# Kernel tuning notes

Hardware: AMD Instinct MI355X
Metric: run time of the kernel (lower is better)

## Reference

```python
import jax, jax.numpy as jnp
import numpy as np

B, T, L = 16, 2048, 512
CH, H_ENC, H_DEC, ATTN_SZ, VOCAB, EMB = 256, 100, 200, 50, 6, 64


def _conv1d(x, k):
    # x: [B,T,Cin], k: [K,Cin,Cout], SAME padding, stride 1
    return jax.lax.conv_general_dilated(x, k, (1,), 'SAME', dimension_numbers=('NWC', 'WIO', 'NWC'))


def _lstm_step(x, c, h, W, b):
    # TF BasicLSTMCell: gates ordered [i, j, f, o], forget_bias = 1.0
    z = jnp.concatenate([x, h], -1) @ W + b
    i, j, f, o = jnp.split(z, 4, -1)
    nc = c * jax.nn.sigmoid(f + 1.0) + jax.nn.sigmoid(i) * jnp.tanh(j)
    nh = jnp.tanh(nc) * jax.nn.sigmoid(o)
    return nc, nh


def _run_lstm(xs, lengths, W, b, hidden):
    # dynamic_rnn semantics: beyond sequence_length, state held, output zeroed
    Bn, Tn, _ = xs.shape
    mask = (jnp.arange(Tn)[:, None] < lengths[None, :])[..., None]  # [T,B,1]

    def step(carry, inp):
        c, h = carry
        x, m = inp
        nc, nh = _lstm_step(x, c, h, W, b)
        c = jnp.where(m, nc, c)
        h = jnp.where(m, nh, h)
        return (c, h), jnp.where(m, nh, 0.0)

    init = (jnp.zeros((Bn, hidden), xs.dtype), jnp.zeros((Bn, hidden), xs.dtype))
    (c, h), outs = jax.lax.scan(step, init, (jnp.swapaxes(xs, 0, 1), mask))
    return jnp.swapaxes(outs, 0, 1), c, h


def _reverse_seq(x, lengths):
    # tf.reverse_sequence along time axis
    t = jnp.arange(x.shape[1])[None, :]
    idx = jnp.where(t < lengths[:, None], lengths[:, None] - 1 - t, t)
    return jnp.take_along_axis(x, idx[..., None], axis=1)


def setup_inputs():
    key = jax.random.key(0)
    ks = jax.random.split(key, 16)
    s = 0.05
    f32 = jnp.float32
    return {
        'signals': jax.random.normal(ks[0], (B, T), f32),
        'embeddings': jax.random.normal(ks[1], (VOCAB, EMB), f32) * s,
        'conv1_k': jax.random.normal(ks[2], (1, 1, CH), f32) * s,
        'conv1a_k': jax.random.normal(ks[3], (1, 1, CH), f32) * s,
        'conv1a_b': jnp.zeros((CH,), f32),
        'conv2_k': jax.random.normal(ks[4], (3, CH, CH), f32) * s,
        'conv3_k': jax.random.normal(ks[5], (1, CH, CH), f32) * s,
        'W_fwd': jax.random.normal(ks[6], (CH + H_ENC, 4 * H_ENC), f32) * s,
        'b_fwd': jnp.zeros((4 * H_ENC,), f32),
        'W_bwd': jax.random.normal(ks[7], (CH + H_ENC, 4 * H_ENC), f32) * s,
        'b_bwd': jnp.zeros((4 * H_ENC,), f32),
        'W_dec': jax.random.normal(ks[8], (EMB + ATTN_SZ + H_DEC, 4 * H_DEC), f32) * s,
        'b_dec': jnp.zeros((4 * H_DEC,), f32),
        'W_mem': jax.random.normal(ks[9], (H_DEC, H_DEC), f32) * s,
        'W_attn': jax.random.normal(ks[10], (2 * H_DEC, ATTN_SZ), f32) * s,
        'W_out': jax.random.normal(ks[11], (ATTN_SZ, VOCAB), f32) * s,
        'labels': jax.random.randint(ks[12], (B, L), 0, 4),
        'sig_length': jax.random.randint(ks[13], (B,), T // 2, T + 1),
        'base_length': jax.random.randint(ks[14], (B,), L // 2, L + 1),
    }


def reference(signals, embeddings, conv1_k, conv1a_k, conv1a_b, conv2_k, conv3_k,
              W_fwd, b_fwd, W_bwd, b_bwd, W_dec, b_dec, W_mem, W_attn, W_out,
              labels, sig_length, base_length):
    # ---- resBlock ----
    x = signals[..., None]                       # [B,T,1]
    c1 = _conv1d(x, conv1_k)                     # no bias
    c1a = _conv1d(x, conv1a_k) + conv1a_b        # with bias (shortcut)
    c3 = _conv1d(_conv1d(c1, conv2_k), conv3_k)
    feat = jax.nn.relu(c3 + c1a)                 # [B,T,256]

    # ---- bidirectional encoder ----
    fwd_out, cf, hf = _run_lstm(feat, sig_length, W_fwd, b_fwd, H_ENC)
    bwd_out, cb, hb = _run_lstm(_reverse_seq(feat, sig_length), sig_length, W_bwd, b_bwd, H_ENC)
    bwd_out = _reverse_seq(bwd_out, sig_length)
    memory = jnp.concatenate([fwd_out, bwd_out], -1)   # [B,T,200]
    c0 = jnp.concatenate([cf, cb], -1)                 # [B,200]
    h0 = jnp.concatenate([hf, hb], -1)

    # ---- Luong attention decoder (teacher forcing) ----
    keys = jnp.einsum('btd,de->bte', memory, W_mem)    # memory_layer (no bias)
    mem_mask = jnp.arange(T)[None, :] < sig_length[:, None]
    neg = jnp.finfo(memory.dtype).min
    emb = embeddings[labels]                            # [B,L,64]

    def dec_step(carry, x_t):
        c, h, attn = carry
        nc, nh = _lstm_step(jnp.concatenate([x_t, attn], -1), c, h, W_dec, b_dec)
        score = jnp.einsum('bd,btd->bt', nh, keys)
        align = jax.nn.softmax(jnp.where(mem_mask, score, neg), axis=-1)
        ctx = jnp.einsum('bt,btd->bd', align, memory)
        new_attn = jnp.concatenate([nh, ctx], -1) @ W_attn   # attention_layer (no bias)
        return (nc, nh, new_attn), new_attn @ W_out          # output Dense(6, no bias)

    attn0 = jnp.zeros((B, ATTN_SZ), memory.dtype)
    _, logits = jax.lax.scan(dec_step, (c0, h0, attn0), jnp.swapaxes(emb, 0, 1))
    logits = jnp.swapaxes(logits, 0, 1)                      # [B,L,6]
    dec_mask = (jnp.arange(L)[None, :] < base_length[:, None])[..., None]
    return jnp.where(dec_mask, logits, jnp.zeros((), logits.dtype))
```

## Files before the change

### kernel.cpp

```cpp
#include <hip/hip_runtime.h>

#define B_ 16
#define T_ 2048
#define L_ 512
#define HD 200
#define AT 50

__device__ __forceinline__ float rcp_(float x){ return __builtin_amdgcn_rcpf(x); }
__device__ __forceinline__ float sigf(float x){ return rcp_(1.f + __expf(-x)); }
__device__ __forceinline__ float tanhf_(float x){
  x = fminf(15.f, fmaxf(-15.f, x));
  float e = __expf(-2.f*x);
  return (1.f - e) * rcp_(1.f + e);
}
__device__ __forceinline__ unsigned bf16u(float v){
  unsigned u = __float_as_uint(v);
  u += 0x7FFFu + ((u >> 16) & 1u);
  return u >> 16;
}
__device__ __forceinline__ unsigned long long pkvs(float v, unsigned s){
  return (unsigned long long)__float_as_uint(v) | ((unsigned long long)s << 32);
}

__global__ void k_prep(const float* __restrict__ conv1, const float* __restrict__ conv1a,
                       const float* __restrict__ conv2, const float* __restrict__ conv3,
                       float* __restrict__ E)
{
  __shared__ float K2s[3*256];
  int tid = threadIdx.x;
  int k = tid >> 8, co = tid & 255;
  float a = 0.f;
  for (int ci = 0; ci < 256; ++ci)
    a = fmaf(conv1[ci], conv2[(k*256 + ci)*256 + co], a);
  K2s[k*256 + co] = a;
  __syncthreads();
  float b2 = 0.f;
  for (int ci = 0; ci < 256; ++ci)
    b2 = fmaf(K2s[k*256 + ci], conv3[ci*256 + co], b2);
  if (k == 1) b2 += conv1a[co];
  E[k*256 + co] = b2;
}

__global__ void k_feat(const float* __restrict__ sig, const float* __restrict__ E,
                       const float* __restrict__ c1ab, float* __restrict__ feat)
{
  int idx = blockIdx.x*256 + threadIdx.x;
  int row = idx >> 6;
  int c4  = (idx & 63) * 4;
  int t = row & (T_-1);
  float sm = (t > 0)     ? sig[row-1] : 0.f;
  float s0 = sig[row];
  float sp = (t < T_-1)  ? sig[row+1] : 0.f;
  float4 e0 = *(const float4*)&E[0*256 + c4];
  float4 e1 = *(const float4*)&E[1*256 + c4];
  float4 e2 = *(const float4*)&E[2*256 + c4];
  float4 bb = *(const float4*)&c1ab[c4];
  float4 r;
  r.x = fmaxf(0.f, fmaf(sm, e0.x, fmaf(s0, e1.x, fmaf(sp, e2.x, bb.x))));
  r.y = fmaxf(0.f, fmaf(sm, e0.y, fmaf(s0, e1.y, fmaf(sp, e2.y, bb.y))));
  r.z = fmaxf(0.f, fmaf(sm, e0.z, fmaf(s0, e1.z, fmaf(sp, e2.z, bb.z))));
  r.w = fmaxf(0.f, fmaf(sm, e0.w, fmaf(s0, e1.w, fmaf(sp, e2.w, bb.w))));
  *(float4*)&feat[(size_t)row*256 + c4] = r;
}

__global__ __launch_bounds__(256)
void k_gemm(const float* __restrict__ A, const float* __restrict__ B,
            const float* __restrict__ bias, float* __restrict__ C,
            int M, int N, int K, int ldb)
{
  __shared__ float As[16][132];
  __shared__ float Bs[16][68];
  int row0 = blockIdx.x*128, col0 = blockIdx.y*64;
  int tid = threadIdx.x;
  int tm = tid >> 4, tn = tid & 15;
  float acc[8][4] = {};
  for (int k0 = 0; k0 < K; k0 += 16){
    #pragma unroll
    for (int i = 0; i < 8; ++i){
      int e = tid + i*256;
      int m = e >> 4, kk = e & 15;
      float v = 0.f;
      if (k0 + kk < K) v = A[(size_t)(row0+m)*K + k0 + kk];
      As[kk][m] = v;
    }
    #pragma unroll
    for (int i = 0; i < 4; ++i){
      int e = tid + i*256;
      int n = e & 63, kb = e >> 6;
      float w = 0.f;
      if (k0 + kb < K && col0 + n < N) w = B[(size_t)(k0+kb)*ldb + col0 + n];
      Bs[kb][n] = w;
    }
    __syncthreads();
    #pragma unroll
    for (int kk = 0; kk < 16; ++kk){
      float a[8], bv[4];
      *(float4*)&a[0] = *(const float4*)&As[kk][tm*8];
      *(float4*)&a[4] = *(const float4*)&As[kk][tm*8+4];
      *(float4*)&bv[0] = *(const float4*)&Bs[kk][tn*4];
      #pragma unroll
      for (int i = 0; i < 8; ++i)
        #pragma unroll
        for (int j = 0; j < 4; ++j)
          acc[i][j] = fmaf(a[i], bv[j], acc[i][j]);
    }
    __syncthreads();
  }
  #pragma unroll
  for (int i = 0; i < 8; ++i){
    int r = row0 + tm*8 + i;
    #pragma unroll
    for (int j = 0; j < 4; ++j){
      int cc = col0 + tn*4 + j;
      if (cc < N) C[(size_t)r*N + cc] = acc[i][j] + (bias ? bias[cc] : 0.f);
    }
  }
}

__global__ void k_permW(const float* __restrict__ Wf, const float* __restrict__ bf,
                        const float* __restrict__ Wb, const float* __restrict__ bb,
                        float* __restrict__ WpF, float* __restrict__ WpB)
{
  int idx = blockIdx.x*256 + threadIdx.x;
  if (idx >= 2*357*400) return;
  int w = idx / (357*400), r = idx - w*(357*400);
  int j = r / 400, col = r - j*400;
  int src = (col & 3)*100 + (col >> 2);
  const float* W = w ? Wb : Wf; const float* bs = w ? bb : bf;
  float v = (j < 356) ? W[j*400 + src] : bs[src];
  (w ? WpB : WpF)[j*400 + col] = v;
}

__global__ __launch_bounds__(512, 1)
void k_encoder(const float* __restrict__ xprojF, const float* __restrict__ xprojB,
               const float* __restrict__ WpF, const float* __restrict__ WpB,
               const int* __restrict__ sig_len, float* __restrict__ memory,
               float* __restrict__ c0h0, int dirParam)
{
  int dir = dirParam, b = blockIdx.x;
  const float* xp = dir ? xprojB : xprojF;
  const float* Wp = dir ? WpB : WpF;
  int tid = threadIdx.x;
  bool act = tid < 400;
  int col = act ? tid : (tid - 400);
  int u = tid >> 2, gq = tid & 3;
  __shared__ __align__(16) float h2[2][104];
  float4 Uv[25];
  #pragma unroll
  for (int j4 = 0; j4 < 25; ++j4){
    Uv[j4].x = Wp[(256 + 4*j4 + 0)*400 + col];
    Uv[j4].y = Wp[(256 + 4*j4 + 1)*400 + col];
    Uv[j4].z = Wp[(256 + 4*j4 + 2)*400 + col];
    Uv[j4].w = Wp[(256 + 4*j4 + 3)*400 + col];
  }
  if (tid < 100) h2[0][tid] = 0.f;
  int len = sig_len[b];
  float c = 0.f, hfin = 0.f;
  int ta = dir ? (len-1) : 0;
  float xb0 = xp[((size_t)(b*T_ + ta))*400 + col];
  int tb_ = dir ? (len-2) : 1;
  float xb1 = xp[((size_t)(b*T_ + tb_))*400 + col];
  for (int step = 0; step < len; ++step){
    __syncthreads();
    int tn = dir ? (len-3-step) : (step+2);
    tn = tn < 0 ? 0 : (tn > T_-1 ? T_-1 : tn);
    float xn = xp[((size_t)(b*T_ + tn))*400 + col];
    const float* hb = h2[step & 1];
    float a0 = xb0, a1 = 0.f, a2 = 0.f, a3 = 0.f;
    #pragma unroll
    for (int j4 = 0; j4 < 25; ++j4){
      float4 h4 = *(const float4*)&hb[j4*4];
      a0 = fmaf(h4.x, Uv[j4].x, a0);
      a1 = fmaf(h4.y, Uv[j4].y, a1);
      a2 = fmaf(h4.z, Uv[j4].z, a2);
      a3 = fmaf(h4.w, Uv[j4].w, a3);
    }
    float z = (a0+a1)+(a2+a3);
    float v0 = z, v1 = __shfl_xor(z, 1);
    float v2 = __shfl_xor(v0, 2), v3 = __shfl_xor(v1, 2);
    float tA  = (gq&1) ? v1 : v0, tB  = (gq&1) ? v3 : v2;
    float tA2 = (gq&1) ? v0 : v1, tB2 = (gq&1) ? v2 : v3;
    float zi = (gq&2) ? tB  : tA;
    float zj = (gq&2) ? tB2 : tA2;
    float zf = (gq&2) ? tA  : tB;
    float zo = (gq&2) ? tA2 : tB2;
    c = c*sigf(zf + 1.f) + sigf(zi)*tanhf_(zj);
    float nh = tanhf_(c)*sigf(zo);
    hfin = nh;
    if (act && gq == 0){
      int t = dir ? (len-1-step) : step;
      h2[(step+1)&1][u] = nh;
      memory[((size_t)(b*T_ + t))*200 + dir*100 + u] = nh;
    }
    xb0 = xb1; xb1 = xn;
  }
  if (act && gq == 0){
    c0h0[b*400 + dir*100 + u]       = c;
    c0h0[b*400 + 200 + dir*100 + u] = hfin;
  }
  int total = (T_ - len)*100;
  for (int i = tid; i < total; i += 512){
    int t = len + i/100;
    int k = i - (i/100)*100;
    memory[((size_t)(b*T_ + t))*200 + dir*100 + k] = 0.f;
  }
}

__global__ void k_gather(const float* __restrict__ emb, const int* __restrict__ labels,
                         float* __restrict__ dA)
{
  int idx = blockIdx.x*256 + threadIdx.x;
  int i = idx >> 6, e = idx & 63;
  dA[(size_t)i*64 + e] = emb[labels[i]*64 + e];
}

__global__ void k_dec_init(unsigned long long* __restrict__ nhb,
                           unsigned long long* __restrict__ parts,
                           unsigned* __restrict__ flags, unsigned fval,
                           float* __restrict__ out)
{
  int idx = blockIdx.x*256 + threadIdx.x;
  if (idx < B_*L_*6) out[idx] = 0.f;
  if (idx < B_*HD) nhb[idx] = 0ull;
  if (idx < B_*16*112) parts[idx] = 0ull;
  if (idx < 32) flags[idx] = fval;
}

#define DEC_LDS 141440
#define TCH 128

__global__ __launch_bounds__(512, 1)
void k_fused(const float* __restrict__ xprojF, const float* __restrict__ xprojB,
             const float* __restrict__ WpF, const float* __restrict__ WpB,
             float* __restrict__ memG, float* c0h0,
             const float* __restrict__ W_mem, const float* __restrict__ W_attn,
             const float* __restrict__ decx, const float* __restrict__ W_dec,
             const float* __restrict__ W_out,
             const int* __restrict__ sig_len, const int* __restrict__ base_len,
             unsigned long long* nhb, unsigned long long* partials,
             unsigned* flags, int encInside,
             float* __restrict__ out)
{
  int blk = blockIdx.x;
  int b = (blk & 7) | (((blk >> 3) & 1) << 3);
  int g = blk >> 4;
  int tid = threadIdx.x;
  int u0 = g * 13;
  int nu = (HD - u0 < 13) ? (HD - u0) : 13;
  int t0 = g * TCH;

  extern __shared__ char smem[];
  uint2* keyP  = (uint2*)(smem);
  float* memAL = (float*)(smem + 51616);
  float* Uld   = (float*)(smem + 77216);
  float* Wa1s  = (float*)(smem + 129216);
  float* WoutL = (float*)(smem + 131824);
  float* nhF   = (float*)(smem + 133024);
  float* spL   = (float*)(smem + 133856);
  float* wL    = (float*)(smem + 135904);
  float* cpL   = (float*)(smem + 136416);
  float* apL   = (float*)(smem + 138080);
  float* zp8   = (float*)(smem + 138288);
  float* zpA   = (float*)(smem + 139952);
  float* attnL = (float*)(smem + 140784);
  float* SL    = (float*)(smem + 140992);
  float* ctxR  = (float*)(smem + 141000);
  float* apR   = (float*)(smem + 141208);

  if (encInside && g < 2){
    int dir = g;
    const float* xp = dir ? xprojB : xprojF;
    const float* Wp = dir ? WpB : WpF;
    float* h2 = spL;
    bool act = tid < 400;
    int col = act ? tid : (tid - 400);
    int u = tid >> 2, gq = tid & 3;
    float4 Uv[25];
    #pragma unroll
    for (int j4 = 0; j4 < 25; ++j4){
      Uv[j4].x = Wp[(256 + 4*j4 + 0)*400 + col];
      Uv[j4].y = Wp[(256 + 4*j4 + 1)*400 + col];
      Uv[j4].z = Wp[(256 + 4*j4 + 2)*400 + col];
      Uv[j4].w = Wp[(256 + 4*j4 + 3)*400 + col];
    }
    if (tid < 104) { h2[tid] = 0.f; h2[104 + tid] = 0.f; }
    int len = sig_len[b];
    float c = 0.f, hfin = 0.f;
    int ta = dir ? (len-1) : 0;
    float xb0 = xp[((size_t)(b*T_ + ta))*400 + col];
    int tb_ = dir ? (len-2) : 1;
    float xb1 = xp[((size_t)(b*T_ + tb_))*400 + col];
    for (int step = 0; step < len; ++step){
      __syncthreads();
      int tn = dir ? (len-3-step) : (step+2);
      tn = tn < 0 ? 0 : (tn > T_-1 ? T_-1 : tn);
      float xn = xp[((size_t)(b*T_ + tn))*400 + col];
      const float* hb = h2 + (step & 1)*104;
      float a0 = xb0, a1 = 0.f, a2 = 0.f, a3 = 0.f;
      #pragma unroll
      for (int j4 = 0; j4 < 25; ++j4){
        float4 h4 = *(const float4*)&hb[j4*4];
        a0 = fmaf(h4.x, Uv[j4].x, a0);
        a1 = fmaf(h4.y, Uv[j4].y, a1);
        a2 = fmaf(h4.z, Uv[j4].z, a2);
        a3 = fmaf(h4.w, Uv[j4].w, a3);
      }
      float z = (a0+a1)+(a2+a3);
      float v0 = z, v1 = __shfl_xor(z, 1);
      float v2 = __shfl_xor(v0, 2), v3 = __shfl_xor(v1, 2);
      float tA  = (gq&1) ? v1 : v0, tB  = (gq&1) ? v3 : v2;
      float tA2 = (gq&1) ? v0 : v1, tB2 = (gq&1) ? v2 : v3;
      float zi = (gq&2) ? tB  : tA;
      float zj = (gq&2) ? tB2 : tA2;
      float zf = (gq&2) ? tA  : tB;
      float zo = (gq&2) ? tA2 : tB2;
      c = c*sigf(zf + 1.f) + sigf(zi)*tanhf_(zj);
      float nh = tanhf_(c)*sigf(zo);
      hfin = nh;
      if (act && gq == 0){
        int t = dir ? (len-1-step) : step;
        h2[((step+1)&1)*104 + u] = nh;
        memG[((size_t)(b*T_ + t))*200 + dir*100 + u] = nh;
      }
      xb0 = xb1; xb1 = xn;
    }
    if (act && gq == 0){
      c0h0[b*400 + dir*100 + u]       = c;
      c0h0[b*400 + 200 + dir*100 + u] = hfin;
    }
    int total = (T_ - len)*100;
    for (int i = tid; i < total; i += 512){
      int t = len + i/100;
      int k = i - (i/100)*100;
      memG[((size_t)(b*T_ + t))*200 + dir*100 + k] = 0.f;
    }
    __syncthreads();
    if (tid == 0){
      __builtin_amdgcn_fence(__ATOMIC_RELEASE, "agent");
      __hip_atomic_store(&flags[b*2 + dir], 1u,
                         __ATOMIC_RELAXED, __HIP_MEMORY_SCOPE_AGENT);
    }
  }

  if (encInside){
    if (tid == 0){
      while (__hip_atomic_load(&flags[b*2+0], __ATOMIC_RELAXED, __HIP_MEMORY_SCOPE_AGENT) == 0u)
        __builtin_amdgcn_s_sleep(8);
      while (__hip_atomic_load(&flags[b*2+1], __ATOMIC_RELAXED, __HIP_MEMORY_SCOPE_AGENT) == 0u)
        __builtin_amdgcn_s_sleep(8);
      __builtin_amdgcn_fence(__ATOMIC_ACQUIRE, "agent");
    }
    __syncthreads();
  }

  unsigned* stg = (unsigned*)Uld;
  for (int i = tid; i < TCH*100; i += 512){
    int t = i / 100, p2 = i - (i/100)*100;
    float2 mv = *(const float2*)&memG[((size_t)(b*T_ + t0 + t))*200 + 2*p2];
    stg[i] = bf16u(mv.x) | (bf16u(mv.y) << 16);
  }
  __syncthreads();
  for (int i = tid; i < TCH*50; i += 512){
    int t = i / 50, q = i - (i/50)*50;
    int d = q*4;
    const unsigned* mrow = stg + t*100;
    float ax = 0.f, ay = 0.f, az = 0.f, aw = 0.f;
    for (int p2 = 0; p2 < 100; ++p2){
      unsigned mm = mrow[p2];
      float m0 = __uint_as_float(mm << 16);
      float m1 = __uint_as_float(mm & 0xFFFF0000u);
      float4 w0 = *(const float4*)&W_mem[(size_t)(2*p2)*200 + d];
      float4 w1 = *(const float4*)&W_mem[(size_t)(2*p2+1)*200 + d];
      ax = fmaf(m0, w0.x, fmaf(m1, w1.x, ax));
      ay = fmaf(m0, w0.y, fmaf(m1, w1.y, ay));
      az = fmaf(m0, w0.z, fmaf(m1, w1.z, az));
      aw = fmaf(m0, w0.w, fmaf(m1, w1.w, aw));
    }
    keyP[q*129 + t] = make_uint2(bf16u(ax) | (bf16u(ay) << 16),
                                 bf16u(az) | (bf16u(aw) << 16));
  }
  for (int i = tid; i < TCH*50; i += 512){
    int t = i / 50, d = i - (i/50)*50;
    const unsigned* mrow = stg + t*100;
    float acc = 0.f;
    for (int p2 = 0; p2 < 100; ++p2){
      unsigned mm = mrow[p2];
      float m0 = __uint_as_float(mm << 16);
      float m1 = __uint_as_float(mm & 0xFFFF0000u);
      acc = fmaf(m0, W_attn[(size_t)(200 + 2*p2)*50 + d],
            fmaf(m1, W_attn[(size_t)(201 + 2*p2)*50 + d], acc));
    }
    memAL[t*50 + d] = acc;
  }
  __syncthreads();

  for (int i = tid; i < 250*52; i += 512){
    int j = i / 52, o_ = i - (i/52)*52;
    int uu = o_ >> 2, gg = o_ & 3;
    Uld[i] = (uu < nu) ? W_dec[(size_t)(64 + j)*800 + gg*200 + u0 + uu] : 0.f;
  }
  for (int i = tid; i < 13*50; i += 512){
    int uw = i / 50, d = i - (i/50)*50;
    Wa1s[i] = (uw < nu) ? W_attn[(size_t)(u0 + uw)*50 + d] : 0.f;
  }
  for (int i = tid; i < 300; i += 512) WoutL[i] = W_out[i];
  if (tid < 52) attnL[tid] = 0.f;
  if (tid < 8)  nhF[200 + tid] = 0.f;
  float creg = (tid < nu) ? c0h0[b*400 + u0 + tid] : 0.f;
  int len = sig_len[b];
  int Lb  = base_len[b];
  unsigned long long* nhB = nhb + (size_t)b*HD;
  __syncthreads();

  if (tid < 50) *(float4*)&nhF[tid*4] = *(const float4*)&c0h0[b*400 + 200 + tid*4];
  __syncthreads();
  int o  = tid - (tid/52)*52;
  int jc8 = tid / 52;
  int jc4 = tid / 52;
  float dcx = 0.f;
  if (tid < 416){
    const float* Ub = &Uld[(50 + jc8*25)*52 + o];
    const float* hp = &nhF[jc8*25];
    float zh = 0.f;
    #pragma unroll
    for (int j = 0; j < 25; ++j) zh = fmaf(hp[j], Ub[(size_t)j*52], zh);
    zp8[o*8 + jc8] = zh;
    if (tid < 52) dcx = decx[((size_t)(b*L_))*800 + (o&3)*200 + u0 + (o>>2)];
  }
  __syncthreads();

  for (int l = 0; l < Lb; ++l){
    unsigned seq = (unsigned)(l + 1);
    if (tid < 208){
      float z = zp8[o*8 + 2*jc4] + zp8[o*8 + 2*jc4 + 1] + ((jc4 == 0) ? dcx : 0.f);
      const float* Ub = &Uld[(jc4*13)*52 + o];
      const float* ap_ = &attnL[jc4*13];
      int cnt = (jc4 < 3) ? 13 : 11;
      for (int j = 0; j < cnt; ++j) z = fmaf(ap_[j], Ub[(size_t)j*52], z);
      zpA[o*4 + jc4] = z;
    } else if (g == 1 && l > 0 && tid >= 208 && tid < 214){
      int j = tid - 208;
      float o_ = 0.f;
      for (int d = 0; d < AT; ++d) o_ = fmaf(attnL[d], WoutL[d*6 + j], o_);
      out[((size_t)(b*L_ + (l-1)))*6 + j] = o_;
    }
    __syncthreads();
    if (tid < nu){
      const float* zz = &zpA[16*tid];
      float zi = (zz[0]+zz[1])+(zz[2]+zz[3]);
      float zj = (zz[4]+zz[5])+(zz[6]+zz[7]);
      float zf = (zz[8]+zz[9])+(zz[10]+zz[11]);
      float zo = (zz[12]+zz[13])+(zz[14]+zz[15]);
      float c = creg;
      c = c*sigf(zf + 1.f) + sigf(zi)*tanhf_(zj);
      creg = c;
      float nh = tanhf_(c)*sigf(zo);
      __hip_atomic_store(&nhB[u0 + tid], pkvs(nh, seq),
                         __ATOMIC_RELAXED, __HIP_MEMORY_SCOPE_AGENT);
    }
    if (tid < HD){
      unsigned long long v;
      do {
        v = __hip_atomic_load(&nhB[tid], __ATOMIC_RELAXED, __HIP_MEMORY_SCOPE_AGENT);
      } while ((unsigned)(v >> 32) != seq);
      nhF[tid] = __uint_as_float((unsigned)v);
    }
    __syncthreads();
    {
      int t = tid & 127, dh = tid >> 7;
      int pstart = (dh < 2) ? dh*13 : 26 + (dh-2)*12;
      int pcnt   = (dh < 2) ? 13 : 12;
      const uint2* kp = &keyP[pstart*129 + t];
      const float4* nf = (const float4*)nhF + pstart;
      float s0 = 0.f, s1 = 0.f;
      for (int q = 0; q < pcnt; ++q){
        uint2 kk = kp[(size_t)q*129];
        float4 nv = nf[q];
        s0 = fmaf(nv.x, __uint_as_float(kk.x << 16), s0);
        s1 = fmaf(nv.y, __uint_as_float(kk.x & 0xFFFF0000u), s1);
        s0 = fmaf(nv.z, __uint_as_float(kk.y << 16), s0);
        s1 = fmaf(nv.w, __uint_as_float(kk.y & 0xFFFF0000u), s1);
      }
      spL[tid] = s0 + s1;
    }
    __syncthreads();
    if (tid < 128){
      float s = (spL[tid] + spL[tid + 128]) + (spL[tid + 256] + spL[tid + 384]);
      float w = 0.f;
      if (t0 + tid < len){ s = fminf(60.f, fmaxf(-60.f, s)); w = __expf(s); }
      wL[tid] = w;
    } else if (tid < 178){
      int d = tid - 128;
      float a = 0.f;
      #pragma unroll
      for (int uw = 0; uw < 13; ++uw) a = fmaf(nhF[u0 + uw], Wa1s[uw*50 + d], a);
      apL[d] = a;
    }
    __syncthreads();
    if (tid >= 448){
      float v = wL[tid - 448] + wL[tid - 384];
      #pragma unroll
      for (int off = 32; off > 0; off >>= 1) v += __shfl_down(v, off);
      if (tid == 448) SL[0] = v;
    } else {
      int tc = tid >> 6, d = tid & 63;
      if (d < 50){
        int tlo = tc*18, thi = (tc == 6) ? 128 : tlo + 18;
        float a = 0.f;
        for (int t = tlo; t < thi; ++t) a = fmaf(wL[t], memAL[t*50 + d], a);
        cpL[tc*52 + d] = a;
      }
    }
    __syncthreads();
    {
      unsigned long long* pb = partials + (size_t)(b*16 + g)*112;
      if (tid < 50){
        float p0 = 0.f;
        #pragma unroll
        for (int k = 0; k < 7; ++k) p0 += cpL[k*52 + tid];
        __hip_atomic_store(&pb[tid], pkvs(p0, seq),
                           __ATOMIC_RELAXED, __HIP_MEMORY_SCOPE_AGENT);
      } else if (tid < 100)
        __hip_atomic_store(&pb[tid], pkvs(apL[tid - 50], seq),
                           __ATOMIC_RELAXED, __HIP_MEMORY_SCOPE_AGENT);
      else if (tid == 100)
        __hip_atomic_store(&pb[100], pkvs(SL[0], seq),
                           __ATOMIC_RELAXED, __HIP_MEMORY_SCOPE_AGENT);
    }
    if (tid < 416){
      const float* Ub = &Uld[(50 + jc8*25)*52 + o];
      const float* hp = &nhF[jc8*25];
      float zh = 0.f;
      #pragma unroll
      for (int j = 0; j < 25; ++j) zh = fmaf(hp[j], Ub[(size_t)j*52], zh);
      zp8[o*8 + jc8] = zh;
      if (tid < 52 && l+1 < Lb)
        dcx = decx[((size_t)(b*L_ + (l+1)))*800 + (o&3)*200 + u0 + (o>>2)];
    }
    if (tid < 101){
      const unsigned long long* base = partials + (size_t)b*16*112 + tid;
      unsigned long long v[16];
      #pragma unroll
      for (int gq2 = 0; gq2 < 16; ++gq2)
        v[gq2] = __hip_atomic_load(&base[gq2*112], __ATOMIC_RELAXED, __HIP_MEMORY_SCOPE_AGENT);
      #pragma unroll
      for (int gq2 = 0; gq2 < 16; ++gq2)
        while ((unsigned)(v[gq2] >> 32) != seq)
          v[gq2] = __hip_atomic_load(&base[gq2*112], __ATOMIC_RELAXED, __HIP_MEMORY_SCOPE_AGENT);
      float acc = 0.f;
      #pragma unroll
      for (int gq2 = 0; gq2 < 16; ++gq2) acc += __uint_as_float((unsigned)v[gq2]);
      if (tid < 50) ctxR[tid] = acc;
      else if (tid < 100) apR[tid - 50] = acc;
      else SL[1] = acc;
    }
    __syncthreads();
    if (tid < 50) attnL[tid] = fmaf(ctxR[tid], rcp_(SL[1]), apR[tid]);
    __syncthreads();
  }
  if (g == 1 && tid < 6){
    float o_ = 0.f;
    for (int d = 0; d < AT; ++d) o_ = fmaf(attnL[d], WoutL[d*6 + tid], o_);
    out[((size_t)(b*L_ + (Lb-1)))*6 + tid] = o_;
  }
}

extern "C" void kernel_launch(void* const* d_in, const int* in_sizes, int n_in,
                              void* d_out, int out_size, void* d_ws, size_t ws_size,
                              hipStream_t stream)
{
  const float* signals   = (const float*)d_in[0];
  const float* embeddings= (const float*)d_in[1];
  const float* conv1_k   = (const float*)d_in[2];
  const float* conv1a_k  = (const float*)d_in[3];
  const float* conv1a_b  = (const float*)d_in[4];
  const float* conv2_k   = (const float*)d_in[5];
  const float* conv3_k   = (const float*)d_in[6];
  const float* W_fwd     = (const float*)d_in[7];
  const float* b_fwd     = (const float*)d_in[8];
  const float* W_bwd     = (const float*)d_in[9];
  const float* b_bwd     = (const float*)d_in[10];
  const float* W_dec     = (const float*)d_in[11];
  const float* b_dec     = (const float*)d_in[12];
  const float* W_mem     = (const float*)d_in[13];
  const float* W_attn    = (const float*)d_in[14];
  const float* W_out     = (const float*)d_in[15];
  const int*   labels    = (const int*)d_in[16];
  const int*   sig_len   = (const int*)d_in[17];
  const int*   base_len  = (const int*)d_in[18];
  float* out = (float*)d_out;
  char* ws = (char*)d_ws;

  const size_t o_c0h0     = 4096;
  const size_t o_nhbuf    = 32768;
  const size_t o_partials = 65536;
  const size_t o_flags    = 458752;
  const size_t o_WpF      = 589824;
  const size_t o_WpB      = 1161024;
  const size_t o_feat     = 4194304;
  const size_t o_mem      = o_feat + 33554432;
  const size_t o_X1       = o_mem + 26214400;
  const size_t o_X2       = o_X1 + 52428800;

  bool bigws = (ws_size >= o_X2 + 52428800);

  float* E      = (float*)(ws);
  float* c0h0   = (float*)(ws + o_c0h0);
  unsigned long long* nhbuf = (unsigned long long*)(ws + o_nhbuf);
  unsigned long long* parts = (unsigned long long*)(ws + o_partials);
  unsigned* flags = (unsigned*)(ws + o_flags);
  float* WpF    = (float*)(ws + o_WpF);
  float* WpB    = (float*)(ws + o_WpB);
  float* feat   = (float*)(ws + o_feat);
  float* memory = (float*)(ws + o_mem);
  float* xprojF = (float*)(ws + o_X1);
  float* xprojB = bigws ? (float*)(ws + o_X2) : xprojF;
  float* decxA  = (float*)(ws + o_feat);
  float* decx   = (float*)(ws + o_feat + 4194304);

  k_prep<<<1, 768, 0, stream>>>(conv1_k, conv1a_k, conv2_k, conv3_k, E);
  k_feat<<<8192, 256, 0, stream>>>(signals, E, conv1a_b, feat);
  k_permW<<<1116, 256, 0, stream>>>(W_fwd, b_fwd, W_bwd, b_bwd, WpF, WpB);

  dim3 gx(256, 7);
  if (bigws){
    k_gemm<<<gx, 256, 0, stream>>>(feat, WpF, WpF + 356*400, xprojF, 32768, 400, 256, 400);
    k_gemm<<<gx, 256, 0, stream>>>(feat, WpB, WpB + 356*400, xprojB, 32768, 400, 256, 400);
  } else {
    k_gemm<<<gx, 256, 0, stream>>>(feat, WpF, WpF + 356*400, xprojF, 32768, 400, 256, 400);
    k_encoder<<<16, 512, 0, stream>>>(xprojF, xprojF, WpF, WpB, sig_len, memory, c0h0, 0);
    k_gemm<<<gx, 256, 0, stream>>>(feat, WpB, WpB + 356*400, xprojF, 32768, 400, 256, 400);
    k_encoder<<<16, 512, 0, stream>>>(xprojF, xprojF, WpF, WpB, sig_len, memory, c0h0, 1);
  }

  k_gather<<<2048, 256, 0, stream>>>(embeddings, labels, decxA);
  k_gemm<<<dim3(64, 13), 256, 0, stream>>>(decxA, W_dec, b_dec, decx, 8192, 800, 64, 800);
  k_dec_init<<<192, 256, 0, stream>>>(nhbuf, parts, flags, bigws ? 0u : 1u, out);

  hipFuncSetAttribute(reinterpret_cast<const void*>(k_fused),
                      hipFuncAttributeMaxDynamicSharedMemorySize, DEC_LDS);
  k_fused<<<256, 512, DEC_LDS, stream>>>(xprojF, xprojB, WpF, WpB,
                                         memory, c0h0, W_mem, W_attn,
                                         decx, W_dec, W_out,
                                         sig_len, base_len,
                                         nhbuf, parts, flags, bigws ? 1 : 0,
                                         out);
}
```

Measured before the change: 4.342 ms.

## Restructure decoder cross-block waits into single wavefronts and remove a barrier

The decoder's cross-block polling for the new hidden state and the attention partials is confined to the first wavefront. That wavefront gathers ctx, attention-projection and softmax-sum partials itself and reduces the sum with shuffles, which removes one block-wide barrier per decode step. The recurrent z-partial buffers are transposed to avoid LDS bank conflicts. The output dense is split across 60 threads, the encoder input prefetch is deepened from 2 to 4 steps, and polling loops add s_sleep to cut memory traffic. In exchange, one wavefront serialises more loads, and the sleep may add latency to the cross-block handoff.

```diff
diff --git a/kernel.cpp b/kernel.cpp
--- a/kernel.cpp
+++ b/kernel.cpp
@@ -20,6 +20,9 @@
 }
 __device__ __forceinline__ unsigned long long pkvs(float v, unsigned s){
   return (unsigned long long)__float_as_uint(v) | ((unsigned long long)s << 32);
+}
+__device__ __forceinline__ unsigned long long ldU64(const unsigned long long* p){
+  return __hip_atomic_load(p, __ATOMIC_RELAXED, __HIP_MEMORY_SCOPE_AGENT);
 }
 
 __global__ void k_prep(const float* __restrict__ conv1, const float* __restrict__ conv1a,
@@ -260,12 +263,11 @@
   float* wL    = (float*)(smem + 135904);
   float* cpL   = (float*)(smem + 136416);
   float* apL   = (float*)(smem + 138080);
-  float* zp8   = (float*)(smem + 138288);
-  float* zpA   = (float*)(smem + 139952);
-  float* attnL = (float*)(smem + 140784);
-  float* SL    = (float*)(smem + 140992);
-  float* ctxR  = (float*)(smem + 141000);
-  float* apR   = (float*)(smem + 141208);
+  float* zp8T  = (float*)(smem + 138288);
+  float* zpAT  = (float*)(smem + 140080);
+  float* attnL = (float*)(smem + 140976);
+  float* SL    = (float*)(smem + 141184);
+  float* opart = (float*)(smem + 141192);
 
   if (encInside && g < 2){
     int dir = g;
@@ -286,17 +288,22 @@
     if (tid < 104) { h2[tid] = 0.f; h2[104 + tid] = 0.f; }
     int len = sig_len[b];
     float c = 0.f, hfin = 0.f;
-    int ta = dir ? (len-1) : 0;
-    float xb0 = xp[((size_t)(b*T_ + ta))*400 + col];
-    int tb_ = dir ? (len-2) : 1;
-    float xb1 = xp[((size_t)(b*T_ + tb_))*400 + col];
+    int tP;
+    tP = dir ? (len-1) : 0; tP = tP < 0 ? 0 : (tP > T_-1 ? T_-1 : tP);
+    float xq0 = xp[((size_t)(b*T_ + tP))*400 + col];
+    tP = dir ? (len-2) : 1; tP = tP < 0 ? 0 : (tP > T_-1 ? T_-1 : tP);
+    float xq1 = xp[((size_t)(b*T_ + tP))*400 + col];
+    tP = dir ? (len-3) : 2; tP = tP < 0 ? 0 : (tP > T_-1 ? T_-1 : tP);
+    float xq2 = xp[((size_t)(b*T_ + tP))*400 + col];
+    tP = dir ? (len-4) : 3; tP = tP < 0 ? 0 : (tP > T_-1 ? T_-1 : tP);
+    float xq3 = xp[((size_t)(b*T_ + tP))*400 + col];
     for (int step = 0; step < len; ++step){
       __syncthreads();
-      int tn = dir ? (len-3-step) : (step+2);
+      int tn = dir ? (len-5-step) : (step+4);
       tn = tn < 0 ? 0 : (tn > T_-1 ? T_-1 : tn);
       float xn = xp[((size_t)(b*T_ + tn))*400 + col];
       const float* hb = h2 + (step & 1)*104;
-      float a0 = xb0, a1 = 0.f, a2 = 0.f, a3 = 0.f;
+      float a0 = xq0, a1 = 0.f, a2 = 0.f, a3 = 0.f;
       #pragma unroll
       for (int j4 = 0; j4 < 25; ++j4){
         float4 h4 = *(const float4*)&hb[j4*4];
@@ -322,7 +329,7 @@
         h2[((step+1)&1)*104 + u] = nh;
         memG[((size_t)(b*T_ + t))*200 + dir*100 + u] = nh;
       }
-      xb0 = xb1; xb1 = xn;
+      xq0 = xq1; xq1 = xq2; xq2 = xq3; xq3 = xn;
     }
     if (act && gq == 0){
       c0h0[b*400 + dir*100 + u]       = c;
@@ -414,56 +421,72 @@
 
   if (tid < 50) *(float4*)&nhF[tid*4] = *(const float4*)&c0h0[b*400 + 200 + tid*4];
   __syncthreads();
-  int o  = tid - (tid/52)*52;
-  int jc8 = tid / 52;
-  int jc4 = tid / 52;
   float dcx = 0.f;
-  if (tid < 416){
-    const float* Ub = &Uld[(50 + jc8*25)*52 + o];
-    const float* hp = &nhF[jc8*25];
+  if (tid >= 96){
+    int i = tid - 96;
+    int o_ = i - (i/52)*52, j8 = i/52;
+    const float* Ub = &Uld[(50 + j8*25)*52 + o_];
+    const float* hp = &nhF[j8*25];
     float zh = 0.f;
     #pragma unroll
     for (int j = 0; j < 25; ++j) zh = fmaf(hp[j], Ub[(size_t)j*52], zh);
-    zp8[o*8 + jc8] = zh;
-    if (tid < 52) dcx = decx[((size_t)(b*L_))*800 + (o&3)*200 + u0 + (o>>2)];
-  }
+    zp8T[j8*56 + o_] = zh;
+  }
+  if (tid < 52)
+    dcx = decx[((size_t)(b*L_))*800 + (tid&3)*200 + u0 + (tid>>2)];
   __syncthreads();
 
   for (int l = 0; l < Lb; ++l){
     unsigned seq = (unsigned)(l + 1);
     if (tid < 208){
-      float z = zp8[o*8 + 2*jc4] + zp8[o*8 + 2*jc4 + 1] + ((jc4 == 0) ? dcx : 0.f);
-      const float* Ub = &Uld[(jc4*13)*52 + o];
+      int o_ = tid - (tid/52)*52, jc4 = tid/52;
+      float z = zp8T[(2*jc4)*56 + o_] + zp8T[(2*jc4+1)*56 + o_] + ((jc4 == 0) ? dcx : 0.f);
+      const float* Ub = &Uld[(jc4*13)*52 + o_];
       const float* ap_ = &attnL[jc4*13];
       int cnt = (jc4 < 3) ? 13 : 11;
       for (int j = 0; j < cnt; ++j) z = fmaf(ap_[j], Ub[(size_t)j*52], z);
-      zpA[o*4 + jc4] = z;
-    } else if (g == 1 && l > 0 && tid >= 208 && tid < 214){
-      int j = tid - 208;
-      float o_ = 0.f;
-      for (int d = 0; d < AT; ++d) o_ = fmaf(attnL[d], WoutL[d*6 + j], o_);
-      out[((size_t)(b*L_ + (l-1)))*6 + j] = o_;
+      zpAT[jc4*56 + o_] = z;
+    } else if (g == 1 && l > 0 && tid >= 256 && tid < 316){
+      int i = tid - 256, j = i - (i/6)*6, k = i/6;
+      float s = 0.f;
+      #pragma unroll
+      for (int d = 0; d < 5; ++d) s = fmaf(attnL[k*5 + d], WoutL[(k*5 + d)*6 + j], s);
+      opart[i] = s;
     }
     __syncthreads();
     if (tid < nu){
-      const float* zz = &zpA[16*tid];
-      float zi = (zz[0]+zz[1])+(zz[2]+zz[3]);
-      float zj = (zz[4]+zz[5])+(zz[6]+zz[7]);
-      float zf = (zz[8]+zz[9])+(zz[10]+zz[11]);
-      float zo = (zz[12]+zz[13])+(zz[14]+zz[15]);
+      int c0 = tid*4;
+      float zi = zpAT[c0  ] + zpAT[56+c0  ] + zpAT[112+c0  ] + zpAT[168+c0  ];
+      float zj = zpAT[c0+1] + zpAT[56+c0+1] + zpAT[112+c0+1] + zpAT[168+c0+1];
+      float zf = zpAT[c0+2] + zpAT[56+c0+2] + zpAT[112+c0+2] + zpAT[168+c0+2];
+      float zo = zpAT[c0+3] + zpAT[56+c0+3] + zpAT[112+c0+3] + zpAT[168+c0+3];
       float c = creg;
       c = c*sigf(zf + 1.f) + sigf(zi)*tanhf_(zj);
       creg = c;
       float nh = tanhf_(c)*sigf(zo);
       __hip_atomic_store(&nhB[u0 + tid], pkvs(nh, seq),
                          __ATOMIC_RELAXED, __HIP_MEMORY_SCOPE_AGENT);
-    }
-    if (tid < HD){
-      unsigned long long v;
-      do {
-        v = __hip_atomic_load(&nhB[tid], __ATOMIC_RELAXED, __HIP_MEMORY_SCOPE_AGENT);
-      } while ((unsigned)(v >> 32) != seq);
-      nhF[tid] = __uint_as_float((unsigned)v);
+    } else if (g == 1 && l > 0 && tid >= 64 && tid < 70){
+      int j = tid - 64;
+      float o_ = 0.f;
+      #pragma unroll
+      for (int k = 0; k < 10; ++k) o_ += opart[k*6 + j];
+      out[((size_t)(b*L_ + (l-1)))*6 + j] = o_;
+    }
+    if (tid < 64){
+      unsigned long long v0 = ldU64(&nhB[tid]);
+      unsigned long long v1 = ldU64(&nhB[tid + 64]);
+      unsigned long long v2 = ldU64(&nhB[tid + 128]);
+      unsigned long long v3 = (tid < 8) ? ldU64(&nhB[tid + 192]) : 0ull;
+      while ((unsigned)(v0 >> 32) != seq){ __builtin_amdgcn_s_sleep(1); v0 = ldU64(&nhB[tid]); }
+      while ((unsigned)(v1 >> 32) != seq){ __builtin_amdgcn_s_sleep(1); v1 = ldU64(&nhB[tid + 64]); }
+      while ((unsigned)(v2 >> 32) != seq){ __builtin_amdgcn_s_sleep(1); v2 = ldU64(&nhB[tid + 128]); }
+      if (tid < 8)
+        while ((unsigned)(v3 >> 32) != seq){ __builtin_amdgcn_s_sleep(1); v3 = ldU64(&nhB[tid + 192]); }
+      nhF[tid]       = __uint_as_float((unsigned)v0);
+      nhF[tid + 64]  = __uint_as_float((unsigned)v1);
+      nhF[tid + 128] = __uint_as_float((unsigned)v2);
+      if (tid < 8) nhF[tid + 192] = __uint_as_float((unsigned)v3);
     }
     __syncthreads();
     {
@@ -514,48 +537,64 @@
     __syncthreads();
     {
       unsigned long long* pb = partials + (size_t)(b*16 + g)*112;
-      if (tid < 50){
-        float p0 = 0.f;
-        #pragma unroll
-        for (int k = 0; k < 7; ++k) p0 += cpL[k*52 + tid];
-        __hip_atomic_store(&pb[tid], pkvs(p0, seq),
+      if (tid < 101){
+        float p;
+        if (tid < 50){
+          p = 0.f;
+          #pragma unroll
+          for (int k = 0; k < 7; ++k) p += cpL[k*52 + tid];
+        } else if (tid < 100) p = apL[tid - 50];
+        else p = SL[0];
+        __hip_atomic_store(&pb[tid], pkvs(p, seq),
                            __ATOMIC_RELAXED, __HIP_MEMORY_SCOPE_AGENT);
-      } else if (tid < 100)
-        __hip_atomic_store(&pb[tid], pkvs(apL[tid - 50], seq),
-                           __ATOMIC_RELAXED, __HIP_MEMORY_SCOPE_AGENT);
-      else if (tid == 100)
-        __hip_atomic_store(&pb[100], pkvs(SL[0], seq),
-                           __ATOMIC_RELAXED, __HIP_MEMORY_SCOPE_AGENT);
-    }
-    if (tid < 416){
-      const float* Ub = &Uld[(50 + jc8*25)*52 + o];
-      const float* hp = &nhF[jc8*25];
+      }
+    }
+    if (tid < 52 && l+1 < Lb)
+      dcx = decx[((size_t)(b*L_ + (l+1)))*800 + (tid&3)*200 + u0 + (tid>>2)];
+    if (tid >= 96){
+      int i = tid - 96;
+      int o_ = i - (i/52)*52, j8 = i/52;
+      const float* Ub = &Uld[(50 + j8*25)*52 + o_];
+      const float* hp = &nhF[j8*25];
       float zh = 0.f;
       #pragma unroll
       for (int j = 0; j < 25; ++j) zh = fmaf(hp[j], Ub[(size_t)j*52], zh);
-      zp8[o*8 + jc8] = zh;
-      if (tid < 52 && l+1 < Lb)
-        dcx = decx[((size_t)(b*L_ + (l+1)))*800 + (o&3)*200 + u0 + (o>>2)];
-    }
-    if (tid < 101){
-      const unsigned long long* base = partials + (size_t)b*16*112 + tid;
-      unsigned long long v[16];
-      #pragma unroll
-      for (int gq2 = 0; gq2 < 16; ++gq2)
-        v[gq2] = __hip_atomic_load(&base[gq2*112], __ATOMIC_RELAXED, __HIP_MEMORY_SCOPE_AGENT);
-      #pragma unroll
-      for (int gq2 = 0; gq2 < 16; ++gq2)
-        while ((unsigned)(v[gq2] >> 32) != seq)
-          v[gq2] = __hip_atomic_load(&base[gq2*112], __ATOMIC_RELAXED, __HIP_MEMORY_SCOPE_AGENT);
-      float acc = 0.f;
-      #pragma unroll
-      for (int gq2 = 0; gq2 < 16; ++gq2) acc += __uint_as_float((unsigned)v[gq2]);
-      if (tid < 50) ctxR[tid] = acc;
-      else if (tid < 100) apR[tid - 50] = acc;
-      else SL[1] = acc;
-    }
-    __syncthreads();
-    if (tid < 50) attnL[tid] = fmaf(ctxR[tid], rcp_(SL[1]), apR[tid]);
+      zp8T[j8*56 + o_] = zh;
+    }
+    if (tid < 50){
+      const unsigned long long* pbB = partials + (size_t)b*16*112;
+      unsigned long long vc[16], va[16];
+      #pragma unroll
+      for (int g2 = 0; g2 < 16; ++g2){
+        vc[g2] = ldU64(&pbB[g2*112 + tid]);
+        va[g2] = ldU64(&pbB[g2*112 + 50 + tid]);
+      }
+      unsigned long long vs = (tid < 16) ? ldU64(&pbB[tid*112 + 100]) : 0ull;
+      #pragma unroll
+      for (int g2 = 0; g2 < 16; ++g2){
+        while ((unsigned)(vc[g2] >> 32) != seq){
+          __builtin_amdgcn_s_sleep(1); vc[g2] = ldU64(&pbB[g2*112 + tid]);
+        }
+        while ((unsigned)(va[g2] >> 32) != seq){
+          __builtin_amdgcn_s_sleep(1); va[g2] = ldU64(&pbB[g2*112 + 50 + tid]);
+        }
+      }
+      if (tid < 16)
+        while ((unsigned)(vs >> 32) != seq){
+          __builtin_amdgcn_s_sleep(1); vs = ldU64(&pbB[tid*112 + 100]);
+        }
+      float sp = (tid < 16) ? __uint_as_float((unsigned)vs) : 0.f;
+      sp += __shfl_xor(sp, 1); sp += __shfl_xor(sp, 2);
+      sp += __shfl_xor(sp, 4); sp += __shfl_xor(sp, 8);
+      float ss = __shfl(sp, 0);
+      float sc = 0.f, sa = 0.f;
+      #pragma unroll
+      for (int g2 = 0; g2 < 16; ++g2){
+        sc += __uint_as_float((unsigned)vc[g2]);
+        sa += __uint_as_float((unsigned)va[g2]);
+      }
+      attnL[tid] = fmaf(sc, rcp_(ss), sa);
+    }
     __syncthreads();
   }
   if (g == 1 && tid < 6){
```

Measured after the change: 6.133 ms. 41.3% more time.
